# Performance work log

Hardware: AMD Instinct MI355X
Metric: run time of the kernel (lower is better)

## Reference

```python
import jax, jax.numpy as jnp
import numpy as np


def setup_inputs() -> dict:
    key = jax.random.key(0)
    k1, k2, k3, k4 = jax.random.split(key, 4)
    n, L, h = 512, 257, 256
    l = L - 1
    hidden, n_labels = 256, 50
    feat = jax.random.normal(k1, (n, L, h), dtype=jnp.float32)
    heads = jax.random.randint(k2, (n, l), 0, L, dtype=jnp.int64)
    masks = jnp.ones((n, l), dtype=jnp.float32)
    # torch nn.Linear layout: (out_features, in_features); xavier-normal-ish scale
    W1 = jax.random.normal(k3, (hidden, 2 * h), dtype=jnp.float32) * (2.0 / (hidden + 2 * h)) ** 0.5
    b1 = jnp.zeros((hidden,), dtype=jnp.float32)
    W2 = jax.random.normal(k4, (n_labels, hidden), dtype=jnp.float32) * (2.0 / (n_labels + hidden)) ** 0.5
    b2 = jnp.zeros((n_labels,), dtype=jnp.float32)
    return {"feat": feat, "heads": heads, "masks": masks,
            "W1": W1, "b1": b1, "W2": W2, "b2": b2}


def reference(feat, heads, masks, W1, b1, W2, b2):
    # feat: (n, L, h); heads: (n, l) with l = L-1, values in [0, L)
    dependent_f = feat[:, 1:, :]                                   # (n, l, h)
    # head_f[b, i] = feat[b, heads[b, i]]  (the gather)
    head_f = jnp.take_along_axis(feat, heads[:, :, None], axis=1)   # (n, l, h)
    cat_f = jnp.concatenate((dependent_f, head_f), axis=2)          # (n, l, 2h)
    hid = jax.nn.relu(jnp.einsum('nlh,oh->nlo', cat_f, W1) + b1)    # (n, l, hidden); dropout is identity at eval
    label_f = jnp.einsum('nlo,ko->nlk', hid, W2) + b2               # (n, l, n_labels)
    return label_f
```

## Files before the change

### kernel.cpp

```cpp
#include <hip/hip_runtime.h>
#include <hip/hip_bf16.h>
#include <stdint.h>

#define AS1 __attribute__((address_space(1)))
#define AS3 __attribute__((address_space(3)))

typedef __bf16 bf16x8 __attribute__((ext_vector_type(8)));
typedef __bf16 bf16x4 __attribute__((ext_vector_type(4)));
typedef float  floatx4 __attribute__((ext_vector_type(4)));

static constexpr int LL   = 257;
static constexpr int HH   = 256;
static constexpr int M    = 131072;
static constexpr int K1   = 512;
static constexpr int NLAB = 50;

#define MFMA_ACC(ACC, A, B) \
  asm("v_mfma_f32_16x16x32_bf16 %0, %1, %2, %0" : "+a"(ACC) : "v"(A), "v"(B))

template<int IMM>
__device__ __forceinline__ floatx4 gload4i(const float* p) {
  floatx4 v;
  asm volatile("global_load_dwordx4 %0, %1, off offset:%2"
               : "=v"(v) : "v"(p), "i"(IMM) : "memory");
  return v;
}

__device__ __forceinline__ bf16x8 cvt8(floatx4 a, floatx4 b) {
  bf16x8 v;
  v[0]=(__bf16)a[0]; v[1]=(__bf16)a[1]; v[2]=(__bf16)a[2]; v[3]=(__bf16)a[3];
  v[4]=(__bf16)b[0]; v[5]=(__bf16)b[1]; v[6]=(__bf16)b[2]; v[7]=(__bf16)b[3];
  return v;
}

__global__ void prep_w(const float* __restrict__ W1, const float* __restrict__ W2,
                       __bf16* __restrict__ w1bt, __bf16* __restrict__ w2b) {
  int idx = blockIdx.x * 256 + threadIdx.x;
  if (idx < 16384) {
    int o  = idx >> 6;
    int kc = idx & 63;
    const float4* s = (const float4*)(W1 + (size_t)o * K1 + kc * 8);
    float4 a = s[0], b = s[1];
    bf16x8 v;
    v[0]=(__bf16)a.x; v[1]=(__bf16)a.y; v[2]=(__bf16)a.z; v[3]=(__bf16)a.w;
    v[4]=(__bf16)b.x; v[5]=(__bf16)b.y; v[6]=(__bf16)b.z; v[7]=(__bf16)b.w;
    *(bf16x8*)(w1bt + ((size_t)(kc * 256 + o)) * 8) = v;
  } else {
    int j = idx - 16384;
    int row = j >> 5;
    int col = (j & 31) * 8;
    float4 a = {0.f,0.f,0.f,0.f}, b = {0.f,0.f,0.f,0.f};
    if (row < NLAB) {
      const float4* s = (const float4*)(W2 + (size_t)row * 256 + col);
      a = s[0]; b = s[1];
    }
    bf16x8 v;
    v[0]=(__bf16)a.x; v[1]=(__bf16)a.y; v[2]=(__bf16)a.z; v[3]=(__bf16)a.w;
    v[4]=(__bf16)b.x; v[5]=(__bf16)b.y; v[6]=(__bf16)b.z; v[7]=(__bf16)b.w;
    *(bf16x8*)(w2b + (size_t)j * 8) = v;
  }
}

template<int KT>
__device__ __forceinline__ void kstep(
    floatx4 (&catP)[3][2], floatx4 (&afc)[4], floatx4 (&afn)[4],
    floatx4 (&acc)[4][4],
    const float* depP, const float* headP,
    const __bf16* afBase, const __bf16* catS, int bbOff, __bf16* catW0) {

  if constexpr (KT < 15) {
    const __bf16* afp = afBase + (KT + 1) * 8192;
    afn[0] = gload4i<0>((const float*)afp);
    afn[1] = gload4i<256>((const float*)afp);
    afn[2] = gload4i<512>((const float*)afp);
    afn[3] = gload4i<768>((const float*)afp);
  }
  if constexpr (KT <= 12) {
    constexpr int CT  = KT + 3;
    constexpr int OFF = (CT & 7) * 128;
    const float* p = (CT < 8) ? depP : headP;
    catP[KT % 3][0] = gload4i<OFF>(p);
    catP[KT % 3][1] = gload4i<OFF + 16>(p);
  }

  floatx4 (&cs)[2] = catP[(KT + 1) % 3];
  if constexpr (KT <= 12)
    asm volatile("s_waitcnt vmcnt(8)" : "+v"(afc[0]),"+v"(afc[1]),"+v"(afc[2]),"+v"(afc[3]),
                                        "+v"(cs[0]),"+v"(cs[1]));
  else if constexpr (KT == 13)
    asm volatile("s_waitcnt vmcnt(6)" : "+v"(afc[0]),"+v"(afc[1]),"+v"(afc[2]),"+v"(afc[3]),
                                        "+v"(cs[0]),"+v"(cs[1]));
  else if constexpr (KT == 14)
    asm volatile("s_waitcnt vmcnt(4)" : "+v"(afc[0]),"+v"(afc[1]),"+v"(afc[2]),"+v"(afc[3]),
                                        "+v"(cs[0]),"+v"(cs[1]));
  else
    asm volatile("s_waitcnt vmcnt(0)"  : "+v"(afc[0]),"+v"(afc[1]),"+v"(afc[2]),"+v"(afc[3]),
                                         "+v"(cs[0]),"+v"(cs[1]));

  const __bf16* crd = catS + (KT & 1) * 2048 + bbOff;
  bf16x8 bb[4];
  #pragma unroll
  for (int mi = 0; mi < 4; ++mi)
    bb[mi] = *(const bf16x8*)(crd + mi * 512);
  #pragma unroll
  for (int oi = 0; oi < 4; ++oi) {
    bf16x8 a = __builtin_bit_cast(bf16x8, afc[oi]);
    #pragma unroll
    for (int mi = 0; mi < 4; ++mi)
      MFMA_ACC(acc[oi][mi], a, bb[mi]);
  }

  if constexpr (KT < 15) {
    __bf16* cw = catW0 + ((KT + 1) & 1) * 2048;
    *(bf16x8*)cw = cvt8(cs[0], cs[1]);
    __builtin_amdgcn_sched_barrier(0);
    asm volatile("s_waitcnt lgkmcnt(0)" ::: "memory");
    __builtin_amdgcn_s_barrier();
    __builtin_amdgcn_sched_barrier(0);
  }
}

__global__ __launch_bounds__(256, 2)
void fused_kernel(const float* __restrict__ feat, const int* __restrict__ heads,
                  const __bf16* __restrict__ w1bt, const float* __restrict__ b1,
                  const __bf16* __restrict__ w2b, const float* __restrict__ b2,
                  float* __restrict__ out) {
  __shared__ __align__(16) char smem[32768];
  __bf16* catS = (__bf16*)smem;
  __bf16* hidS = (__bf16*)smem;

  const int t    = threadIdx.x;
  const int w    = t >> 6;
  const int lane = t & 63;
  const int lr   = lane & 15;
  const int q    = lane >> 4;
  const int mBase = blockIdx.x * 64;

  const int r = t >> 2;
  const int c = t & 3;
  const int m0 = mBase + r;
  const int seq = m0 >> 8;
  const float* depP  = feat + ((size_t)(seq * LL + (m0 & 255) + 1)) * HH + c * 8;
  const float* headP = feat + ((size_t)(seq * LL + heads[m0])) * HH + c * 8;
  asm volatile("" : "+v"(headP));

  const int pos0 = r * 4 + (c ^ ((r >> 1) & 3));
  __bf16* catW0 = catS + pos0 * 8;
  const int bbOff = lr * 32 + (q ^ ((lr >> 1) & 3)) * 8;
  const __bf16* afBase = w1bt + ((size_t)(q * 256 + w * 64 + lr)) * 8;

  floatx4 acc[4][4];
  #pragma unroll
  for (int i = 0; i < 4; ++i)
    #pragma unroll
    for (int j = 0; j < 4; ++j)
      acc[i][j] = (floatx4){0.f, 0.f, 0.f, 0.f};

  floatx4 catP[3][2];
  floatx4 afA[4], afB[4];

  catP[0][0] = gload4i<0>(depP);    catP[0][1] = gload4i<16>(depP);
  catP[1][0] = gload4i<128>(depP);  catP[1][1] = gload4i<144>(depP);
  afA[0] = gload4i<0>((const float*)afBase);
  afA[1] = gload4i<256>((const float*)afBase);
  afA[2] = gload4i<512>((const float*)afBase);
  afA[3] = gload4i<768>((const float*)afBase);
  catP[2][0] = gload4i<256>(depP);  catP[2][1] = gload4i<272>(depP);
  asm volatile("s_waitcnt vmcnt(8)" : "+v"(catP[0][0]),"+v"(catP[0][1]));
  *(bf16x8*)catW0 = cvt8(catP[0][0], catP[0][1]);
  __builtin_amdgcn_sched_barrier(0);
  asm volatile("s_waitcnt lgkmcnt(0)" ::: "memory");
  __builtin_amdgcn_s_barrier();
  __builtin_amdgcn_sched_barrier(0);

  kstep< 0>(catP, afA, afB, acc, depP, headP, afBase, catS, bbOff, catW0);
  kstep< 1>(catP, afB, afA, acc, depP, headP, afBase, catS, bbOff, catW0);
  kstep< 2>(catP, afA, afB, acc, depP, headP, afBase, catS, bbOff, catW0);
  kstep< 3>(catP, afB, afA, acc, depP, headP, afBase, catS, bbOff, catW0);
  kstep< 4>(catP, afA, afB, acc, depP, headP, afBase, catS, bbOff, catW0);
  kstep< 5>(catP, afB, afA, acc, depP, headP, afBase, catS, bbOff, catW0);
  kstep< 6>(catP, afA, afB, acc, depP, headP, afBase, catS, bbOff, catW0);
  kstep< 7>(catP, afB, afA, acc, depP, headP, afBase, catS, bbOff, catW0);
  kstep< 8>(catP, afA, afB, acc, depP, headP, afBase, catS, bbOff, catW0);
  kstep< 9>(catP, afB, afA, acc, depP, headP, afBase, catS, bbOff, catW0);
  kstep<10>(catP, afA, afB, acc, depP, headP, afBase, catS, bbOff, catW0);
  kstep<11>(catP, afB, afA, acc, depP, headP, afBase, catS, bbOff, catW0);
  kstep<12>(catP, afA, afB, acc, depP, headP, afBase, catS, bbOff, catW0);
  kstep<13>(catP, afB, afA, acc, depP, headP, afBase, catS, bbOff, catW0);
  kstep<14>(catP, afA, afB, acc, depP, headP, afBase, catS, bbOff, catW0);
  kstep<15>(catP, afB, afA, acc, depP, headP, afBase, catS, bbOff, catW0);

  __syncthreads();

  float4 biasv[4];
  #pragma unroll
  for (int oi = 0; oi < 4; ++oi)
    biasv[oi] = *(const float4*)(b1 + w * 64 + oi * 16 + q * 4);

  #pragma unroll
  for (int mi = 0; mi < 4; ++mi) {
    const int mr = mi * 16 + lr;
    const int s  = lr & 7;
    #pragma unroll
    for (int oi = 0; oi < 4; ++oi) {
      const int cj = w * 8 + oi * 2 + (q >> 1);
      bf16x4 hv;
      const float* bp = (const float*)&biasv[oi];
      #pragma unroll
      for (int rr = 0; rr < 4; ++rr) {
        float v = acc[oi][mi][rr] + bp[rr];
        v = v > 0.f ? v : 0.f;
        hv[rr] = (__bf16)v;
      }
      *(bf16x4*)(hidS + mr * 256 + ((cj ^ s) << 3) + (q & 1) * 4) = hv;
    }
  }
  __syncthreads();

  bf16x8 w2f[8];
  #pragma unroll
  for (int kt2 = 0; kt2 < 8; ++kt2)
    w2f[kt2] = *(const bf16x8*)(w2b + (size_t)(w * 16 + lr) * 256 + kt2 * 32 + q * 8);

  floatx4 acc2[4];
  #pragma unroll
  for (int i = 0; i < 4; ++i) acc2[i] = (floatx4){0.f, 0.f, 0.f, 0.f};

  #pragma unroll
  for (int kt2 = 0; kt2 < 8; ++kt2) {
    const int gc = kt2 * 4 + q;
    #pragma unroll
    for (int mi = 0; mi < 4; ++mi) {
      bf16x8 a2 = *(const bf16x8*)(hidS + (mi * 16 + lr) * 256 + ((gc ^ (lr & 7)) << 3));
      acc2[mi] = __builtin_amdgcn_mfma_f32_16x16x32_bf16(a2, w2f[kt2], acc2[mi], 0, 0, 0);
    }
  }
  __syncthreads();

  float* outT = (float*)smem;
  const int col = w * 16 + lr;
  if (col < NLAB) {
    const float bias = b2[col];
    #pragma unroll
    for (int mi = 0; mi < 4; ++mi) {
      const int rowB = mi * 16 + q * 4;
      #pragma unroll
      for (int rr = 0; rr < 4; ++rr)
        outT[(rowB + rr) * NLAB + col] = acc2[mi][rr] + bias;
    }
  }
  __syncthreads();

  float* odst = out + (size_t)mBase * NLAB;
  #pragma unroll
  for (int i = t; i < 800; i += 256)
    *(float4*)(odst + i * 4) = *(const float4*)(outT + i * 4);
}

extern "C" void kernel_launch(void* const* d_in, const int* in_sizes, int n_in,
                              void* d_out, int out_size, void* d_ws, size_t ws_size,
                              hipStream_t stream) {
  const float* feat  = (const float*)d_in[0];
  const int*   heads = (const int*)d_in[1];
  const float* W1 = (const float*)d_in[3];
  const float* b1 = (const float*)d_in[4];
  const float* W2 = (const float*)d_in[5];
  const float* b2 = (const float*)d_in[6];
  float* out = (float*)d_out;

  __bf16* w1bt = (__bf16*)d_ws;
  __bf16* w2b  = w1bt + 256 * 512;

  prep_w<<<72, 256, 0, stream>>>(W1, W2, w1bt, w2b);
  fused_kernel<<<M / 64, 256, 0, stream>>>(feat, heads, w1bt, b1, w2b, b2, out);
}
```

Before: 239.0 us.

## Stage full concatenated activation tile in LDS upfront, drop per-step barriers

Replaces the per-k-step streaming of feature rows (with hand-written waitcnts and a barrier every step) with an up-front load of the whole 64x512 concatenated tile into 64KB of LDS, then one barrier. The K loop then needs no barriers and uses compiler-scheduled loads, with a triple-buffered W1 prefetch two steps ahead. Doubling LDS to 64KB may cut occupancy from two blocks per CU. It also serializes all global loads before any MFMA work, losing overlap within a block.

```diff
diff --git a/kernel.cpp b/kernel.cpp
--- a/kernel.cpp
+++ b/kernel.cpp
@@ -1,9 +1,6 @@
 #include <hip/hip_runtime.h>
 #include <hip/hip_bf16.h>
 #include <stdint.h>
-
-#define AS1 __attribute__((address_space(1)))
-#define AS3 __attribute__((address_space(3)))
 
 typedef __bf16 bf16x8 __attribute__((ext_vector_type(8)));
 typedef __bf16 bf16x4 __attribute__((ext_vector_type(4)));
@@ -14,17 +11,6 @@
 static constexpr int M    = 131072;
 static constexpr int K1   = 512;
 static constexpr int NLAB = 50;
-
-#define MFMA_ACC(ACC, A, B) \
-  asm("v_mfma_f32_16x16x32_bf16 %0, %1, %2, %0" : "+a"(ACC) : "v"(A), "v"(B))
-
-template<int IMM>
-__device__ __forceinline__ floatx4 gload4i(const float* p) {
-  floatx4 v;
-  asm volatile("global_load_dwordx4 %0, %1, off offset:%2"
-               : "=v"(v) : "v"(p), "i"(IMM) : "memory");
-  return v;
-}
 
 __device__ __forceinline__ bf16x8 cvt8(floatx4 a, floatx4 b) {
   bf16x8 v;
@@ -63,61 +49,26 @@
 
 template<int KT>
 __device__ __forceinline__ void kstep(
-    floatx4 (&catP)[3][2], floatx4 (&afc)[4], floatx4 (&afn)[4],
-    floatx4 (&acc)[4][4],
-    const float* depP, const float* headP,
-    const __bf16* afBase, const __bf16* catS, int bbOff, __bf16* catW0) {
-
-  if constexpr (KT < 15) {
-    const __bf16* afp = afBase + (KT + 1) * 8192;
-    afn[0] = gload4i<0>((const float*)afp);
-    afn[1] = gload4i<256>((const float*)afp);
-    afn[2] = gload4i<512>((const float*)afp);
-    afn[3] = gload4i<768>((const float*)afp);
-  }
-  if constexpr (KT <= 12) {
-    constexpr int CT  = KT + 3;
-    constexpr int OFF = (CT & 7) * 128;
-    const float* p = (CT < 8) ? depP : headP;
-    catP[KT % 3][0] = gload4i<OFF>(p);
-    catP[KT % 3][1] = gload4i<OFF + 16>(p);
-  }
-
-  floatx4 (&cs)[2] = catP[(KT + 1) % 3];
-  if constexpr (KT <= 12)
-    asm volatile("s_waitcnt vmcnt(8)" : "+v"(afc[0]),"+v"(afc[1]),"+v"(afc[2]),"+v"(afc[3]),
-                                        "+v"(cs[0]),"+v"(cs[1]));
-  else if constexpr (KT == 13)
-    asm volatile("s_waitcnt vmcnt(6)" : "+v"(afc[0]),"+v"(afc[1]),"+v"(afc[2]),"+v"(afc[3]),
-                                        "+v"(cs[0]),"+v"(cs[1]));
-  else if constexpr (KT == 14)
-    asm volatile("s_waitcnt vmcnt(4)" : "+v"(afc[0]),"+v"(afc[1]),"+v"(afc[2]),"+v"(afc[3]),
-                                        "+v"(cs[0]),"+v"(cs[1]));
-  else
-    asm volatile("s_waitcnt vmcnt(0)"  : "+v"(afc[0]),"+v"(afc[1]),"+v"(afc[2]),"+v"(afc[3]),
-                                         "+v"(cs[0]),"+v"(cs[1]));
-
-  const __bf16* crd = catS + (KT & 1) * 2048 + bbOff;
+    bf16x8 (&afc)[4], bf16x8 (&afi)[4], floatx4 (&acc)[4][4],
+    const __bf16* afBase, const __bf16* catS, int bbOff) {
+
+  if constexpr (KT < 14) {
+    const __bf16* afp = afBase + (KT + 2) * 8192;
+    #pragma unroll
+    for (int oi = 0; oi < 4; ++oi)
+      afi[oi] = *(const bf16x8*)(afp + oi * 128);
+  }
+
+  const __bf16* crd = catS + KT * 2048 + bbOff;
   bf16x8 bb[4];
   #pragma unroll
   for (int mi = 0; mi < 4; ++mi)
     bb[mi] = *(const bf16x8*)(crd + mi * 512);
   #pragma unroll
-  for (int oi = 0; oi < 4; ++oi) {
-    bf16x8 a = __builtin_bit_cast(bf16x8, afc[oi]);
+  for (int oi = 0; oi < 4; ++oi)
     #pragma unroll
     for (int mi = 0; mi < 4; ++mi)
-      MFMA_ACC(acc[oi][mi], a, bb[mi]);
-  }
-
-  if constexpr (KT < 15) {
-    __bf16* cw = catW0 + ((KT + 1) & 1) * 2048;
-    *(bf16x8*)cw = cvt8(cs[0], cs[1]);
-    __builtin_amdgcn_sched_barrier(0);
-    asm volatile("s_waitcnt lgkmcnt(0)" ::: "memory");
-    __builtin_amdgcn_s_barrier();
-    __builtin_amdgcn_sched_barrier(0);
-  }
+      acc[oi][mi] = __builtin_amdgcn_mfma_f32_16x16x32_bf16(afc[oi], bb[mi], acc[oi][mi], 0, 0, 0);
 }
 
 __global__ __launch_bounds__(256, 2)
@@ -125,7 +76,7 @@
                   const __bf16* __restrict__ w1bt, const float* __restrict__ b1,
                   const __bf16* __restrict__ w2b, const float* __restrict__ b2,
                   float* __restrict__ out) {
-  __shared__ __align__(16) char smem[32768];
+  __shared__ __align__(16) char smem[65536];
   __bf16* catS = (__bf16*)smem;
   __bf16* hidS = (__bf16*)smem;
 
@@ -134,18 +85,36 @@
   const int lane = t & 63;
   const int lr   = lane & 15;
   const int q    = lane >> 4;
+
   const int mBase = blockIdx.x * 64;
 
-  const int r = t >> 2;
-  const int c = t & 3;
-  const int m0 = mBase + r;
-  const int seq = m0 >> 8;
-  const float* depP  = feat + ((size_t)(seq * LL + (m0 & 255) + 1)) * HH + c * 8;
-  const float* headP = feat + ((size_t)(seq * LL + heads[m0])) * HH + c * 8;
-  asm volatile("" : "+v"(headP));
-
-  const int pos0 = r * 4 + (c ^ ((r >> 1) & 3));
-  __bf16* catW0 = catS + pos0 * 8;
+  const int inrow   = t & 7;
+  const int rowslot = t >> 3;
+  const int seq     = mBase >> 8;
+  const int mA      = mBase + rowslot;
+  const int mB      = mBase + 32 + rowslot;
+  const float* rp[4];
+  rp[0] = feat + ((size_t)(seq * LL + (mA & 255) + 1)) * HH + inrow * 8;
+  rp[1] = feat + ((size_t)(seq * LL + (mB & 255) + 1)) * HH + inrow * 8;
+  rp[2] = feat + ((size_t)(seq * LL + heads[mA])) * HH + inrow * 8;
+  rp[3] = feat + ((size_t)(seq * LL + heads[mB])) * HH + inrow * 8;
+
+  #pragma unroll
+  for (int g = 0; g < 4; ++g) {
+    const int r = (g & 1) * 32 + rowslot;
+    const int kbase = (g >= 2) ? 32 : 0;
+    #pragma unroll
+    for (int s = 0; s < 4; ++s) {
+      floatx4 a = *(const floatx4*)(rp[g] + s * 64);
+      floatx4 b = *(const floatx4*)(rp[g] + s * 64 + 4);
+      const int ko  = kbase + s * 8 + inrow;
+      const int kt  = ko >> 2;
+      const int c   = ko & 3;
+      const int pos = r * 4 + (c ^ ((r >> 1) & 3));
+      *(bf16x8*)(catS + kt * 2048 + pos * 8) = cvt8(a, b);
+    }
+  }
+
   const int bbOff = lr * 32 + (q ^ ((lr >> 1) & 3)) * 8;
   const __bf16* afBase = w1bt + ((size_t)(q * 256 + w * 64 + lr)) * 8;
 
@@ -156,39 +125,30 @@
     for (int j = 0; j < 4; ++j)
       acc[i][j] = (floatx4){0.f, 0.f, 0.f, 0.f};
 
-  floatx4 catP[3][2];
-  floatx4 afA[4], afB[4];
-
-  catP[0][0] = gload4i<0>(depP);    catP[0][1] = gload4i<16>(depP);
-  catP[1][0] = gload4i<128>(depP);  catP[1][1] = gload4i<144>(depP);
-  afA[0] = gload4i<0>((const float*)afBase);
-  afA[1] = gload4i<256>((const float*)afBase);
-  afA[2] = gload4i<512>((const float*)afBase);
-  afA[3] = gload4i<768>((const float*)afBase);
-  catP[2][0] = gload4i<256>(depP);  catP[2][1] = gload4i<272>(depP);
-  asm volatile("s_waitcnt vmcnt(8)" : "+v"(catP[0][0]),"+v"(catP[0][1]));
-  *(bf16x8*)catW0 = cvt8(catP[0][0], catP[0][1]);
-  __builtin_amdgcn_sched_barrier(0);
-  asm volatile("s_waitcnt lgkmcnt(0)" ::: "memory");
-  __builtin_amdgcn_s_barrier();
-  __builtin_amdgcn_sched_barrier(0);
-
-  kstep< 0>(catP, afA, afB, acc, depP, headP, afBase, catS, bbOff, catW0);
-  kstep< 1>(catP, afB, afA, acc, depP, headP, afBase, catS, bbOff, catW0);
-  kstep< 2>(catP, afA, afB, acc, depP, headP, afBase, catS, bbOff, catW0);
-  kstep< 3>(catP, afB, afA, acc, depP, headP, afBase, catS, bbOff, catW0);
-  kstep< 4>(catP, afA, afB, acc, depP, headP, afBase, catS, bbOff, catW0);
-  kstep< 5>(catP, afB, afA, acc, depP, headP, afBase, catS, bbOff, catW0);
-  kstep< 6>(catP, afA, afB, acc, depP, headP, afBase, catS, bbOff, catW0);
-  kstep< 7>(catP, afB, afA, acc, depP, headP, afBase, catS, bbOff, catW0);
-  kstep< 8>(catP, afA, afB, acc, depP, headP, afBase, catS, bbOff, catW0);
-  kstep< 9>(catP, afB, afA, acc, depP, headP, afBase, catS, bbOff, catW0);
-  kstep<10>(catP, afA, afB, acc, depP, headP, afBase, catS, bbOff, catW0);
-  kstep<11>(catP, afB, afA, acc, depP, headP, afBase, catS, bbOff, catW0);
-  kstep<12>(catP, afA, afB, acc, depP, headP, afBase, catS, bbOff, catW0);
-  kstep<13>(catP, afB, afA, acc, depP, headP, afBase, catS, bbOff, catW0);
-  kstep<14>(catP, afA, afB, acc, depP, headP, afBase, catS, bbOff, catW0);
-  kstep<15>(catP, afB, afA, acc, depP, headP, afBase, catS, bbOff, catW0);
+  bf16x8 a0[4], a1[4], a2[4];
+  #pragma unroll
+  for (int oi = 0; oi < 4; ++oi) a0[oi] = *(const bf16x8*)(afBase + oi * 128);
+  #pragma unroll
+  for (int oi = 0; oi < 4; ++oi) a1[oi] = *(const bf16x8*)(afBase + 8192 + oi * 128);
+
+  __syncthreads();
+
+  kstep< 0>(a0, a2, acc, afBase, catS, bbOff);
+  kstep< 1>(a1, a0, acc, afBase, catS, bbOff);
+  kstep< 2>(a2, a1, acc, afBase, catS, bbOff);
+  kstep< 3>(a0, a2, acc, afBase, catS, bbOff);
+  kstep< 4>(a1, a0, acc, afBase, catS, bbOff);
+  kstep< 5>(a2, a1, acc, afBase, catS, bbOff);
+  kstep< 6>(a0, a2, acc, afBase, catS, bbOff);
+  kstep< 7>(a1, a0, acc, afBase, catS, bbOff);
+  kstep< 8>(a2, a1, acc, afBase, catS, bbOff);
+  kstep< 9>(a0, a2, acc, afBase, catS, bbOff);
+  kstep<10>(a1, a0, acc, afBase, catS, bbOff);
+  kstep<11>(a2, a1, acc, afBase, catS, bbOff);
+  kstep<12>(a0, a2, acc, afBase, catS, bbOff);
+  kstep<13>(a1, a0, acc, afBase, catS, bbOff);
+  kstep<14>(a2, a1, acc, afBase, catS, bbOff);
+  kstep<15>(a0, a2, acc, afBase, catS, bbOff);
 
   __syncthreads();
 
@@ -231,8 +191,8 @@
     const int gc = kt2 * 4 + q;
     #pragma unroll
     for (int mi = 0; mi < 4; ++mi) {
-      bf16x8 a2 = *(const bf16x8*)(hidS + (mi * 16 + lr) * 256 + ((gc ^ (lr & 7)) << 3));
-      acc2[mi] = __builtin_amdgcn_mfma_f32_16x16x32_bf16(a2, w2f[kt2], acc2[mi], 0, 0, 0);
+      bf16x8 a2f = *(const bf16x8*)(hidS + (mi * 16 + lr) * 256 + ((gc ^ (lr & 7)) << 3));
+      acc2[mi] = __builtin_amdgcn_mfma_f32_16x16x32_bf16(a2f, w2f[kt2], acc2[mi], 0, 0, 0);
     }
   }
   __syncthreads();
```

After: 248.9 us. +4.2%, slower.
